# Optimization experiments

Measured on AMD Instinct MI355X. Metric: run time of the kernel, lower is better.

Reference implementation:

```python
import jax, jax.numpy as jnp
import numpy as np
from jax import lax

HEADS = 8
WIN_SIZES = (2, 4, 8)


def _linear(x, w, b):
    return x @ w + b


def _window_attention(x2d, ws, w4, b4):
    # x2d: (B,H,W,C); w4: (4,C,C) = [q,k,v,out]; b4: (4,C)
    B, H, W, C = x2d.shape
    p1, p2 = H // ws, W // ws
    xw = x2d.reshape(B, p1, ws, p2, ws, C).transpose(0, 1, 3, 2, 4, 5)
    xw = xw.reshape(B, p1, p2, ws * ws, C)
    hs = C // HEADS
    q = _linear(xw, w4[0], b4[0]).reshape(B, p1, p2, ws * ws, HEADS, hs)
    k = _linear(xw, w4[1], b4[1]).reshape(B, p1, p2, ws * ws, HEADS, hs)
    v = _linear(xw, w4[2], b4[2]).reshape(B, p1, p2, ws * ws, HEADS, hs)
    scores = jnp.einsum('bpqwhd,bpqvhd->bpqhwv', q, k) / jnp.sqrt(jnp.asarray(hs, x2d.dtype))
    probs = jax.nn.softmax(scores, axis=-1)
    ctx = jnp.einsum('bpqhwv,bpqvhd->bpqwhd', probs, v).reshape(B, p1, p2, ws * ws, C)
    return _linear(ctx, w4[3], b4[3])


def _unwindow(out, ws):
    B, p1, p2, win, C = out.shape
    s = out.reshape(B, p1, p2, ws, ws, C).transpose(0, 1, 3, 2, 4, 5)
    return s.reshape(B, p1 * ws, p2 * ws, C)


def _up_bilinear_ac(x, oh, ow):
    # x: (B,C,h,w); bilinear with align_corners=True (UpsamplingBilinear2d)
    B, C, h, w = x.shape
    def grid(o, i):
        pos = jnp.arange(o, dtype=x.dtype) * ((i - 1) / (o - 1))
        i0 = jnp.floor(pos).astype(jnp.int32)
        i1 = jnp.minimum(i0 + 1, i - 1)
        return i0, i1, pos - i0.astype(x.dtype)
    r0, r1, tr = grid(oh, h)
    c0, c1, tc = grid(ow, w)
    xr = x[:, :, r0, :] * (1 - tr)[None, None, :, None] + x[:, :, r1, :] * tr[None, None, :, None]
    return xr[:, :, :, c0] * (1 - tc) + xr[:, :, :, c1] * tc


def _forward(x, attn_w, attn_b, edge_w, mlp_w1, mlp_b1, mlp_w2, mlp_b2,
             dl_w, dl_b, ax_w, ax_b, g_shift, g_bias, sq_w, sq_b):
    B, N, C = x.shape
    H = W = int(np.sqrt(N))
    x2d = x.reshape(B, H, W, C)

    # multi-scale window attention branches
    scale_outputs = [_unwindow(_window_attention(x2d, ws, attn_w[i], attn_b[i]), ws)
                     for i, ws in enumerate(WIN_SIZES)]

    # adaptive window selector
    xc = x2d.transpose(0, 3, 1, 2)  # (B,C,H,W)
    edge = jnp.abs(lax.conv_general_dilated(xc, edge_w, (1, 1), 'SAME'))
    avg = lax.reduce_window(edge, 0.0, lax.add, (1, 1, 3, 3), (1, 1, 1, 1), 'SAME') / 9.0
    e = avg.transpose(0, 2, 3, 1)  # (B,H,W,1)
    wts = jax.nn.softmax(jax.nn.relu(e @ mlp_w1 + mlp_b1) @ mlp_w2 + mlp_b2, axis=-1)

    blended = sum(wts[..., i:i + 1] * scale_outputs[i] for i in range(len(WIN_SIZES)))
    h_map = blended.transpose(0, 3, 1, 2)  # (B,C,H,W)

    # ws=4 window attention -> DlightConv token pooling
    x_win = _window_attention(x2d, 4, attn_w[1], attn_b[1])  # (B,p,p,16,C)
    probs = jax.nn.softmax(jnp.mean(x_win, axis=-2) @ dl_w + dl_b, axis=-1)
    x_dl = jnp.sum(x_win * probs[..., None], axis=-2)  # (B,p,p,C)

    # axial attention (no head split, no scaling in the axial branch)
    q = _linear(x_dl, ax_w[0], ax_b[0])
    k = _linear(x_dl, ax_w[1], ax_b[1])
    v = _linear(x_dl, ax_w[2], ax_b[2])
    scores_x = jnp.einsum('bhwc,bhvc->bhwv', q, k)  # (B,r,c,k)
    scores_y = jnp.einsum('bhwc,bvwc->bwhv', q, k)  # (B,c,r,k)

    # GaussianTrans: vectorized per-pixel gaussian positional bias
    p = x_dl.shape[1]
    idx = jnp.arange(p, dtype=x.dtype)
    dist2 = (idx[None, :] - idx[:, None]) ** 2          # [pos, k]
    gb = -(g_shift[0] * dist2 + g_bias[0])              # (p,p)
    ax = jax.nn.softmax(scores_x + gb[None, None, :, :], axis=-1)       # bias indexed by c
    ay = jax.nn.softmax(jnp.swapaxes(scores_y, 1, 2) + gb[None, :, None, :], axis=-1)  # bias by r
    x_g = jnp.einsum('brck,brkd->brcd', ax, v) + jnp.einsum('brck,bkcd->brcd', ay, v)

    x_g = _up_bilinear_ac(x_g.transpose(0, 3, 1, 2), H, W)  # (B,C,H,W)

    cat = jnp.concatenate([x_g, h_map], axis=1)  # (B,2C,H,W)
    out = jnp.einsum('oc,bchw->bohw', sq_w, cat) + sq_b[None, :, None, None]
    return out.transpose(0, 2, 3, 1).reshape(B, N, C)


def setup_inputs() -> dict:
    key = jax.random.key(0)
    ks = jax.random.split(key, 16)
    B, N, C = 16, 4096, 256
    s = 0.02
    return {
        'x': jax.random.normal(ks[0], (B, N, C), jnp.float32),
        'attn_w': jax.random.normal(ks[1], (3, 4, C, C), jnp.float32) * s,
        'attn_b': jax.random.normal(ks[2], (3, 4, C), jnp.float32) * s,
        'edge_w': jax.random.normal(ks[3], (1, C, 3, 3), jnp.float32) * s,
        'mlp_w1': jax.random.normal(ks[4], (1, 16), jnp.float32) * s,
        'mlp_b1': jax.random.normal(ks[5], (16,), jnp.float32) * s,
        'mlp_w2': jax.random.normal(ks[6], (16, 3), jnp.float32) * s,
        'mlp_b2': jax.random.normal(ks[7], (3,), jnp.float32) * s,
        'dl_w': jax.random.normal(ks[8], (C, 16), jnp.float32) * s,
        'dl_b': jax.random.normal(ks[9], (16,), jnp.float32) * s,
        'ax_w': jax.random.normal(ks[10], (3, C, C), jnp.float32) * s,
        'ax_b': jax.random.normal(ks[11], (3, C), jnp.float32) * s,
        'g_shift': jnp.abs(jax.random.normal(ks[12], (1,), jnp.float32)),
        'g_bias': -jnp.abs(jax.random.normal(ks[13], (1,), jnp.float32)),
        'sq_w': jax.random.normal(ks[14], (C, 2 * C), jnp.float32) * s,
        'sq_b': jax.random.normal(ks[15], (C,), jnp.float32) * s,
    }


def reference(x, attn_w, attn_b, edge_w, mlp_w1, mlp_b1, mlp_w2, mlp_b2,
              dl_w, dl_b, ax_w, ax_b, g_shift, g_bias, sq_w, sq_b):
    return _forward(x, attn_w, attn_b, edge_w, mlp_w1, mlp_b1, mlp_w2, mlp_b2,
                    dl_w, dl_b, ax_w, ax_b, g_shift, g_bias, sq_w, sq_b)
```

## Files before the change

### kernel.cpp

```cpp
#include <hip/hip_runtime.h>
#include <math.h>


#define CHUNK_B 4
#define CHUNK_TOK (CHUNK_B * 4096)
#define SA 40

typedef __attribute__((ext_vector_type(8))) short short8;
typedef __attribute__((ext_vector_type(4))) float f32x4;

__device__ __forceinline__ ushort f2bf(float f) {
    union { float f; unsigned u; } v; v.f = f;
    unsigned r = v.u + 0x7fff + ((v.u >> 16) & 1);
    return (ushort)(r >> 16);
}
__device__ __forceinline__ float bf2f(ushort h) {
    union { unsigned u; float f; } v; v.u = ((unsigned)h) << 16; return v.f;
}
__device__ __forceinline__ void split2(float v, ushort& h, ushort& l) {
    h = f2bf(v);
    l = f2bf(v - bf2f(h));
}

__global__ __launch_bounds__(256) void split_w_kmajor(
    const float* __restrict__ W, ushort* __restrict__ Th, ushort* __restrict__ Tl, int nmats)
{
    const int idx = blockIdx.x * 256 + threadIdx.x;
    if (idx >= nmats * 65536) return;
    const int mat = idx >> 16, r = idx & 65535;
    const int n = r >> 8, k = r & 255;
    const float v = W[(size_t)mat * 65536 + k * 256 + n];
    ushort h, l; split2(v, h, l);
    Th[idx] = h; Tl[idx] = l;
}
__global__ __launch_bounds__(256) void split_w_nmajor(
    const float* __restrict__ W, ushort* __restrict__ Th, ushort* __restrict__ Tl, int total)
{
    const int idx = blockIdx.x * 256 + threadIdx.x;
    if (idx >= total) return;
    ushort h, l; split2(W[idx], h, l);
    Th[idx] = h; Tl[idx] = l;
}


#define GEMM_DECLS                                                            \
    __shared__ ushort Ah[128 * SA], Al[128 * SA], Bh[128 * SA], Bl[128 * SA]; \
    const int tid = threadIdx.x;                                              \
    const int wave = tid >> 6, lane = tid & 63;                               \
    const int quad = lane >> 4, l16 = lane & 15;                              \
    const int wr = (wave >> 1) * 64, wc = (wave & 1) * 64;                    \
    f32x4 acc[4][4];                                                          \
    _Pragma("unroll") for (int i = 0; i < 4; i++)                             \
        _Pragma("unroll") for (int j = 0; j < 4; j++)                         \
            acc[i][j] = (f32x4){0.f, 0.f, 0.f, 0.f};                          \
    const int srow = tid >> 1;                                    \
    const int skp  = (tid & 1) * 16;

#define STAGE_A(Aptr, kk)                                                     \
    {                                                                         \
        const float* src = (Aptr) + (size_t)(m0 + srow) * 256 + (kk) + skp;   \
        _Pragma("unroll") for (int c = 0; c < 4; c++) {                       \
            float4 v = *(const float4*)(src + c * 4);                         \
            ushort4 h, l;                                                     \
            split2(v.x, h.x, l.x); split2(v.y, h.y, l.y);                     \
            split2(v.z, h.z, l.z); split2(v.w, h.w, l.w);                     \
            *(ushort4*)&Ah[srow * SA + skp + c * 4] = h;                      \
            *(ushort4*)&Al[srow * SA + skp + c * 4] = l;                      \
        }                                                                     \
    }

#define STAGE_B(WthP, WtlP, Kst, k0)                                          \
    {                                                                         \
        const size_t wo = (size_t)(srow) * (Kst) + (k0) + skp;                \
        *(ulonglong2*)&Bh[srow * SA + skp]     = *(const ulonglong2*)((WthP) + wo);     \
        *(ulonglong2*)&Bh[srow * SA + skp + 8] = *(const ulonglong2*)((WthP) + wo + 8); \
        *(ulonglong2*)&Bl[srow * SA + skp]     = *(const ulonglong2*)((WtlP) + wo);     \
        *(ulonglong2*)&Bl[srow * SA + skp + 8] = *(const ulonglong2*)((WtlP) + wo + 8); \
    }

#define GEMM_COMPUTE                                                          \
    {                                                                         \
        short8 afh[4], afl[4], bfh[4], bfl[4];                                \
        _Pragma("unroll") for (int i = 0; i < 4; i++) {                       \
            const int ro = (wr + i * 16 + l16) * SA + quad * 8;               \
            afh[i] = *(const short8*)&Ah[ro];                                 \
            afl[i] = *(const short8*)&Al[ro];                                 \
        }                                                                     \
        _Pragma("unroll") for (int j = 0; j < 4; j++) {                       \
            const int no = (wc + j * 16 + l16) * SA + quad * 8;               \
            bfh[j] = *(const short8*)&Bh[no];                                 \
            bfl[j] = *(const short8*)&Bl[no];                                 \
        }                                                                     \
        _Pragma("unroll") for (int i = 0; i < 4; i++)                         \
            _Pragma("unroll") for (int j = 0; j < 4; j++) {                   \
                acc[i][j] = __builtin_amdgcn_mfma_f32_16x16x32_bf16(          \
                    afh[i], bfh[j], acc[i][j], 0, 0, 0);                      \
                acc[i][j] = __builtin_amdgcn_mfma_f32_16x16x32_bf16(          \
                    afl[i], bfh[j], acc[i][j], 0, 0, 0);                      \
                acc[i][j] = __builtin_amdgcn_mfma_f32_16x16x32_bf16(          \
                    afh[i], bfl[j], acc[i][j], 0, 0, 0);                      \
            }                                                                 \
    }

__global__ __launch_bounds__(256, 2) void gemm3_mfma(
    const float* __restrict__ A,
    const ushort* __restrict__ Wth, const ushort* __restrict__ Wtl,
    const float* __restrict__ b0, const float* __restrict__ b1, const float* __restrict__ b2,
    float* __restrict__ O0, float* __restrict__ O1, float* __restrict__ O2)
{
    const int m0 = blockIdx.x * 128;
    const int mat = blockIdx.y >> 1;
    const int col0 = (blockIdx.y & 1) * 128;
    const ushort* wth = Wth + (size_t)mat * 65536 + (size_t)col0 * 256;
    const ushort* wtl = Wtl + (size_t)mat * 65536 + (size_t)col0 * 256;
    GEMM_DECLS
    for (int k0 = 0; k0 < 256; k0 += 32) {
        STAGE_A(A, k0)
        STAGE_B(wth, wtl, 256, k0)
        __syncthreads();
        GEMM_COMPUTE
        __syncthreads();
    }
    const float* bias = (mat == 0) ? b0 : (mat == 1) ? b1 : b2;
    float* O = (mat == 0) ? O0 : (mat == 1) ? O1 : O2;
#pragma unroll
    for (int j = 0; j < 4; j++) {
        const int col = col0 + wc + j * 16 + l16;
        const float bj = bias[col];
#pragma unroll
        for (int i = 0; i < 4; i++) {
            const int rbase = m0 + wr + i * 16 + quad * 4;
#pragma unroll
            for (int r = 0; r < 4; r++)
                O[(size_t)(rbase + r) * 256 + col] = acc[i][j][r] + bj;
        }
    }
}

__global__ __launch_bounds__(256, 2) void gemmp_mfma(
    const float* __restrict__ A,
    const ushort* __restrict__ Wth, const ushort* __restrict__ Wtl,
    const float* __restrict__ bias,
    float* __restrict__ Sout, int store_s,
    float* __restrict__ Blnd, const float* __restrict__ wts, int scale_idx, int blend_init,
    int row_off)
{
    const int m0 = blockIdx.x * 128;
    const int col0 = blockIdx.y * 128;
    const ushort* wth = Wth + (size_t)col0 * 256;
    const ushort* wtl = Wtl + (size_t)col0 * 256;
    GEMM_DECLS
    for (int k0 = 0; k0 < 256; k0 += 32) {
        STAGE_A(A, k0)
        STAGE_B(wth, wtl, 256, k0)
        __syncthreads();
        GEMM_COMPUTE
        __syncthreads();
    }
#pragma unroll
    for (int i = 0; i < 4; i++) {
        const int rbase = m0 + wr + i * 16 + quad * 4;
#pragma unroll
        for (int r = 0; r < 4; r++) {
            const size_t grow = (size_t)row_off + rbase + r;
            const float wt = wts[grow * 3 + scale_idx];
#pragma unroll
            for (int j = 0; j < 4; j++) {
                const int col = col0 + wc + j * 16 + l16;
                const float v = acc[i][j][r] + bias[col];
                if (store_s) Sout[grow * 256 + col] = v;
                float* bp = Blnd + grow * 256 + col;
                if (blend_init) *bp = wt * v;
                else            *bp = *bp + wt * v;
            }
        }
    }
}

__global__ __launch_bounds__(256, 2) void gemmf_mfma(
    const float* __restrict__ UP, const float* __restrict__ BLD,
    const ushort* __restrict__ Wth, const ushort* __restrict__ Wtl,
    const float* __restrict__ SQB, float* __restrict__ OUT)
{
    const int m0 = blockIdx.x * 128;
    const int col0 = blockIdx.y * 128;
    const ushort* wth = Wth + (size_t)col0 * 512;
    const ushort* wtl = Wtl + (size_t)col0 * 512;
    GEMM_DECLS
    for (int k0 = 0; k0 < 512; k0 += 32) {
        const float* Ap = (k0 < 256) ? UP : BLD;
        STAGE_A(Ap, (k0 & 255))
        STAGE_B(wth, wtl, 512, k0)
        __syncthreads();
        GEMM_COMPUTE
        __syncthreads();
    }
#pragma unroll
    for (int j = 0; j < 4; j++) {
        const int col = col0 + wc + j * 16 + l16;
        const float bj = SQB[col];
#pragma unroll
        for (int i = 0; i < 4; i++) {
            const int rbase = m0 + wr + i * 16 + quad * 4;
#pragma unroll
            for (int r = 0; r < 4; r++)
                OUT[(size_t)(rbase + r) * 256 + col] = acc[i][j][r] + bj;
        }
    }
}

template <int WS, int NH>
__global__ __launch_bounds__(256) void win_attn(
    const float* __restrict__ Q, const float* __restrict__ K,
    const float* __restrict__ V, float* __restrict__ CTX)
{
    constexpr int WIN = WS * WS;
    constexpr int NW = 64 / WS;
    constexpr int CW = NH * 32;
    __shared__ float qs[WIN][CW + 4], ks[WIN][CW + 4], vs[WIN][CW + 4];
    __shared__ float sc[NH][WIN][WIN + 1];
    const int tid = threadIdx.x;
    const int wid = blockIdx.x;
    const int b = wid / (NW * NW);
    const int rem = wid % (NW * NW);
    const int p = rem / NW, q = rem % NW;
    const int h0 = blockIdx.y * NH;

    for (int idx = tid; idx < WIN * CW; idx += 256) {
        const int i = idx / CW;
        const int cc = idx % CW;
        const int ti = i / WS, tj = i % WS;
        const size_t g = ((size_t)(b * 4096 + (p * WS + ti) * 64 + (q * WS + tj))) * 256 + h0 * 32 + cc;
        qs[i][cc] = Q[g]; ks[i][cc] = K[g]; vs[i][cc] = V[g];
    }
    __syncthreads();
    const float scale = 0.17677669529663687f;
    for (int idx = tid; idx < NH * WIN * WIN; idx += 256) {
        const int hl = idx / (WIN * WIN);
        const int r = idx % (WIN * WIN);
        const int i = r / WIN, j = r % WIN;
        const int co = hl * 32;
        float s = 0.f;
#pragma unroll
        for (int d = 0; d < 32; d++) s += qs[i][co + d] * ks[j][co + d];
        sc[hl][i][j] = s * scale;
    }
    __syncthreads();
    if (tid < NH * WIN) {
        const int hl = tid / WIN, i = tid % WIN;
        float mx = -3.4e38f;
        for (int j = 0; j < WIN; j++) mx = fmaxf(mx, sc[hl][i][j]);
        float sum = 0.f;
        for (int j = 0; j < WIN; j++) {
            float e = __expf(sc[hl][i][j] - mx);
            sc[hl][i][j] = e; sum += e;
        }
        const float inv = 1.f / sum;
        for (int j = 0; j < WIN; j++) sc[hl][i][j] *= inv;
    }
    __syncthreads();
    for (int idx = tid; idx < WIN * CW; idx += 256) {
        const int i = idx / CW;
        const int cc = idx % CW;
        const int hl = cc >> 5;
        float s = 0.f;
        for (int j = 0; j < WIN; j++) s += sc[hl][i][j] * vs[j][cc];
        const int ti = i / WS, tj = i % WS;
        const size_t g = ((size_t)(b * 4096 + (p * WS + ti) * 64 + (q * WS + tj))) * 256 + h0 * 32 + cc;
        CTX[g] = s;
    }
}

__global__ __launch_bounds__(256) void edge_conv(
    const float* __restrict__ x, const float* __restrict__ ew, float* __restrict__ edge)
{
    __shared__ float wsm[2304];
    __shared__ float red[4];
    const int bh = blockIdx.x;
    const int b = bh >> 6, h = bh & 63;
    const int tid = threadIdx.x;
    for (int i = tid; i < 2304; i += 256) wsm[i] = ew[i];
    __syncthreads();
    float wc[9];
#pragma unroll
    for (int t = 0; t < 9; t++) wc[t] = wsm[tid * 9 + t];

    for (int w = 0; w < 64; w++) {
        float acc = 0.f;
#pragma unroll
        for (int kh = 0; kh < 3; kh++) {
            const int hh = h + kh - 1;
            if ((unsigned)hh > 63u) continue;
#pragma unroll
            for (int kw = 0; kw < 3; kw++) {
                const int ww = w + kw - 1;
                if ((unsigned)ww > 63u) continue;
                acc += x[((size_t)b * 4096 + hh * 64 + ww) * 256 + tid] * wc[kh * 3 + kw];
            }
        }
        for (int off = 32; off; off >>= 1) acc += __shfl_down(acc, off);
        if ((tid & 63) == 0) red[tid >> 6] = acc;
        __syncthreads();
        if (tid == 0)
            edge[(size_t)b * 4096 + h * 64 + w] = fabsf(red[0] + red[1] + red[2] + red[3]);
        __syncthreads();
    }
}

__global__ __launch_bounds__(256) void avg_mlp(
    const float* __restrict__ edge, const float* __restrict__ w1, const float* __restrict__ b1,
    const float* __restrict__ w2, const float* __restrict__ b2, float* __restrict__ wts)
{
    const int idx = blockIdx.x * 256 + threadIdx.x;
    const int b = idx >> 12, rem = idx & 4095, h = rem >> 6, w = rem & 63;
    float s = 0.f;
#pragma unroll
    for (int kh = -1; kh <= 1; kh++) {
        const int hh = h + kh;
        if ((unsigned)hh > 63u) continue;
#pragma unroll
        for (int kw = -1; kw <= 1; kw++) {
            const int ww = w + kw;
            if ((unsigned)ww > 63u) continue;
            s += edge[(size_t)b * 4096 + hh * 64 + ww];
        }
    }
    const float e = s / 9.f;
    float l0 = b2[0], l1 = b2[1], l2 = b2[2];
#pragma unroll
    for (int j = 0; j < 16; j++) {
        float hd = fmaxf(e * w1[j] + b1[j], 0.f);
        l0 += hd * w2[j * 3 + 0];
        l1 += hd * w2[j * 3 + 1];
        l2 += hd * w2[j * 3 + 2];
    }
    const float mx = fmaxf(l0, fmaxf(l1, l2));
    const float e0 = __expf(l0 - mx), e1 = __expf(l1 - mx), e2 = __expf(l2 - mx);
    const float inv = 1.f / (e0 + e1 + e2);
    wts[(size_t)idx * 3 + 0] = e0 * inv;
    wts[(size_t)idx * 3 + 1] = e1 * inv;
    wts[(size_t)idx * 3 + 2] = e2 * inv;
}

__global__ __launch_bounds__(256) void dlight(
    const float* __restrict__ S1, const float* __restrict__ dlw,
    const float* __restrict__ dlb, float* __restrict__ XDL)
{
    __shared__ float xw[16][257];
    __shared__ float m[256];
    __shared__ float pr[16];
    __shared__ float pr2[16];
    const int wid = blockIdx.x;
    const int b = wid >> 8, rem = wid & 255, p = rem >> 4, q = rem & 15;
    const int tid = threadIdx.x;
#pragma unroll
    for (int t = 0; t < 16; t++) {
        const int ti = t >> 2, tj = t & 3;
        xw[t][tid] = S1[((size_t)b * 4096 + (p * 4 + ti) * 64 + (q * 4 + tj)) * 256 + tid];
    }
    float mm = 0.f;
#pragma unroll
    for (int t = 0; t < 16; t++) mm += xw[t][tid];
    m[tid] = mm * (1.f / 16.f);
    __syncthreads();
    if (tid < 16) {
        float lg = dlb[tid];
        for (int c = 0; c < 256; c++) lg += m[c] * dlw[c * 16 + tid];
        pr[tid] = lg;
    }
    __syncthreads();
    if (tid < 16) {
        float mx = -3.4e38f;
        for (int j = 0; j < 16; j++) mx = fmaxf(mx, pr[j]);
        float sum = 0.f;
        for (int j = 0; j < 16; j++) sum += __expf(pr[j] - mx);
        pr2[tid] = __expf(pr[tid] - mx) / sum;
    }
    __syncthreads();
    float o = 0.f;
#pragma unroll
    for (int t = 0; t < 16; t++) o += xw[t][tid] * pr2[t];
    XDL[(size_t)wid * 256 + tid] = o;
}

__global__ __launch_bounds__(256) void axial_row(
    const float* __restrict__ Q, const float* __restrict__ K, const float* __restrict__ V,
    const float* __restrict__ gsp, const float* __restrict__ gbp, float* __restrict__ XG)
{
    __shared__ float qs[16][257], ks[16][257], vs[16][257];
    __shared__ float sc[16][17];
    const int bid = blockIdx.x;
    const int b = bid >> 4, r = bid & 15;
    const int tid = threadIdx.x;
    const float gs = gsp[0], gb = gbp[0];
#pragma unroll
    for (int w = 0; w < 16; w++) {
        const size_t base = ((size_t)b * 256 + r * 16 + w) * 256 + tid;
        qs[w][tid] = Q[base]; ks[w][tid] = K[base]; vs[w][tid] = V[base];
    }
    __syncthreads();
    {
        const int w = tid >> 4, vv = tid & 15;
        float s = 0.f;
        for (int c = 0; c < 256; c++) s += qs[w][c] * ks[vv][c];
        const float d = (float)(w - vv);
        sc[w][vv] = s - (gs * d * d + gb);
    }
    __syncthreads();
    if (tid < 16) {
        float mx = -3.4e38f;
        for (int j = 0; j < 16; j++) mx = fmaxf(mx, sc[tid][j]);
        float sum = 0.f;
        for (int j = 0; j < 16; j++) {
            float e = __expf(sc[tid][j] - mx);
            sc[tid][j] = e; sum += e;
        }
        const float inv = 1.f / sum;
        for (int j = 0; j < 16; j++) sc[tid][j] *= inv;
    }
    __syncthreads();
#pragma unroll
    for (int w2 = 0; w2 < 16; w2++) {
        float o = 0.f;
#pragma unroll
        for (int k2 = 0; k2 < 16; k2++) o += sc[w2][k2] * vs[k2][tid];
        XG[((size_t)b * 256 + r * 16 + w2) * 256 + tid] = o;
    }
}

__global__ __launch_bounds__(256) void axial_col(
    const float* __restrict__ Q, const float* __restrict__ K, const float* __restrict__ V,
    const float* __restrict__ gsp, const float* __restrict__ gbp, float* __restrict__ XG)
{
    __shared__ float qs[16][257], ks[16][257], vs[16][257];
    __shared__ float sc[16][17];
    const int bid = blockIdx.x;
    const int b = bid >> 4, col = bid & 15;
    const int tid = threadIdx.x;
    const float gs = gsp[0], gb = gbp[0];
#pragma unroll
    for (int h = 0; h < 16; h++) {
        const size_t base = ((size_t)b * 256 + h * 16 + col) * 256 + tid;
        qs[h][tid] = Q[base]; ks[h][tid] = K[base]; vs[h][tid] = V[base];
    }
    __syncthreads();
    {
        const int r = tid >> 4, vv = tid & 15;
        float s = 0.f;
        for (int c = 0; c < 256; c++) s += qs[r][c] * ks[vv][c];
        const float d = (float)(r - vv);
        sc[r][vv] = s - (gs * d * d + gb);
    }
    __syncthreads();
    if (tid < 16) {
        float mx = -3.4e38f;
        for (int j = 0; j < 16; j++) mx = fmaxf(mx, sc[tid][j]);
        float sum = 0.f;
        for (int j = 0; j < 16; j++) {
            float e = __expf(sc[tid][j] - mx);
            sc[tid][j] = e; sum += e;
        }
        const float inv = 1.f / sum;
        for (int j = 0; j < 16; j++) sc[tid][j] *= inv;
    }
    __syncthreads();
#pragma unroll
    for (int r2 = 0; r2 < 16; r2++) {
        float o = 0.f;
#pragma unroll
        for (int k2 = 0; k2 < 16; k2++) o += sc[r2][k2] * vs[k2][tid];
        XG[((size_t)b * 256 + r2 * 16 + col) * 256 + tid] += o;
    }
}

__global__ __launch_bounds__(256) void upsample(
    const float* __restrict__ XG, float* __restrict__ UP)
{
    const unsigned idx = blockIdx.x * 256u + threadIdx.x;
    const int c = idx & 255;
    const unsigned t2 = idx >> 8;
    const int w = t2 & 63;
    const unsigned t3 = t2 >> 6;
    const int h = t3 & 63;
    const int b = t3 >> 6;
    const float rr = 15.f / 63.f;
    const float ph = h * rr, pw = w * rr;
    int h0 = (int)floorf(ph); float th = ph - (float)h0; int h1 = min(h0 + 1, 15);
    int w0 = (int)floorf(pw); float tw = pw - (float)w0; int w1 = min(w0 + 1, 15);
    const size_t bb = (size_t)b * 256;
    const float v00 = XG[((bb + h0 * 16 + w0)) * 256 + c];
    const float v10 = XG[((bb + h1 * 16 + w0)) * 256 + c];
    const float v01 = XG[((bb + h0 * 16 + w1)) * 256 + c];
    const float v11 = XG[((bb + h1 * 16 + w1)) * 256 + c];
    const float c0 = v00 * (1.f - th) + v10 * th;
    const float c1 = v01 * (1.f - th) + v11 * th;
    UP[idx] = c0 * (1.f - tw) + c1 * tw;
}

extern "C" void kernel_launch(void* const* d_in, const int* in_sizes, int n_in,
                              void* d_out, int out_size, void* d_ws, size_t ws_size,
                              hipStream_t stream)
{
    const float* x      = (const float*)d_in[0];
    const float* attn_w = (const float*)d_in[1];
    const float* attn_b = (const float*)d_in[2];
    const float* edge_w = (const float*)d_in[3];
    const float* mlp_w1 = (const float*)d_in[4];
    const float* mlp_b1 = (const float*)d_in[5];
    const float* mlp_w2 = (const float*)d_in[6];
    const float* mlp_b2 = (const float*)d_in[7];
    const float* dl_w   = (const float*)d_in[8];
    const float* dl_b   = (const float*)d_in[9];
    const float* ax_w   = (const float*)d_in[10];
    const float* ax_b   = (const float*)d_in[11];
    const float* g_shift= (const float*)d_in[12];
    const float* g_bias = (const float*)d_in[13];
    const float* sq_w   = (const float*)d_in[14];
    const float* sq_b   = (const float*)d_in[15];
    float* out = (float*)d_out;

    float* ws = (float*)d_ws;
    const size_t MT = 65536;
    float* blend = ws;
    float* s1    = blend + MT * 256;
    float* scr   = s1 + MT * 256;
    float* chQ   = scr;
    float* chK   = chQ + (size_t)CHUNK_TOK * 256;
    float* chV   = chK + (size_t)CHUNK_TOK * 256;
    float* up    = scr;
    float* edge  = scr + MT * 256;
    float* wts   = edge + 65536;
    float* xdl   = wts + 196608;
    float* axq   = xdl + 1048576;
    float* axk   = axq + 1048576;
    float* axv   = axk + 1048576;
    float* xg    = axv + 1048576;
    ushort* Wth = (ushort*)(xg + 1048576);
    ushort* Wtl = Wth + 1114112;

    split_w_kmajor<<<(12 * 65536 + 255) / 256, 256, 0, stream>>>(attn_w, Wth, Wtl, 12);
    split_w_kmajor<<<(3 * 65536 + 255) / 256, 256, 0, stream>>>(
        ax_w, Wth + (size_t)12 * 65536, Wtl + (size_t)12 * 65536, 3);
    split_w_nmajor<<<(131072 + 255) / 256, 256, 0, stream>>>(
        sq_w, Wth + (size_t)15 * 65536, Wtl + (size_t)15 * 65536, 131072);

    edge_conv<<<1024, 256, 0, stream>>>(x, edge_w, edge);
    avg_mlp<<<256, 256, 0, stream>>>(edge, mlp_w1, mlp_b1, mlp_w2, mlp_b2, wts);

    for (int i = 0; i < 3; i++) {
        const ushort* Wh = Wth + (size_t)i * 4 * 65536;
        const ushort* Wl = Wtl + (size_t)i * 4 * 65536;
        const float* c0 = attn_b + (size_t)(i * 4 + 0) * 256;
        const float* c1 = attn_b + (size_t)(i * 4 + 1) * 256;
        const float* c2 = attn_b + (size_t)(i * 4 + 2) * 256;
        const float* c3 = attn_b + (size_t)(i * 4 + 3) * 256;
        for (int ch = 0; ch < 16 / CHUNK_B; ch++) {
            const size_t toff = (size_t)ch * CHUNK_TOK;
            const float* xc = x + toff * 256;
            gemm3_mfma<<<dim3(CHUNK_TOK / 128, 6), 256, 0, stream>>>(
                xc, Wh, Wl, c0, c1, c2, chQ, chK, chV);
            if (i == 0)
                win_attn<2, 8><<<dim3(CHUNK_B * 32 * 32, 1), 256, 0, stream>>>(chQ, chK, chV, chQ);
            if (i == 1)
                win_attn<4, 4><<<dim3(CHUNK_B * 16 * 16, 2), 256, 0, stream>>>(chQ, chK, chV, chQ);
            if (i == 2)
                win_attn<8, 1><<<dim3(CHUNK_B * 8 * 8, 8), 256, 0, stream>>>(chQ, chK, chV, chQ);
            gemmp_mfma<<<dim3(CHUNK_TOK / 128, 2), 256, 0, stream>>>(
                chQ, Wh + (size_t)3 * 65536, Wl + (size_t)3 * 65536, c3,
                s1, (i == 1) ? 1 : 0, blend, wts, i, (i == 0) ? 1 : 0, (int)toff);
        }
    }

    dlight<<<4096, 256, 0, stream>>>(s1, dl_w, dl_b, xdl);

    gemm3_mfma<<<dim3(4096 / 128, 6), 256, 0, stream>>>(
        xdl, Wth + (size_t)12 * 65536, Wtl + (size_t)12 * 65536,
        ax_b, ax_b + 256, ax_b + 512, axq, axk, axv);
    axial_row<<<256, 256, 0, stream>>>(axq, axk, axv, g_shift, g_bias, xg);
    axial_col<<<256, 256, 0, stream>>>(axq, axk, axv, g_shift, g_bias, xg);

    upsample<<<65536, 256, 0, stream>>>(xg, up);

    gemmf_mfma<<<dim3(512, 2), 256, 0, stream>>>(
        up, blend, Wth + (size_t)15 * 65536, Wtl + (size_t)15 * 65536, sq_b, out);
}
```

Measured before the change: 1.409 ms.

## Split edge conv into per-pixel channel contraction then 3x3 spatial combine

Replaces the edge-detection conv kernel, which looped over 64 columns per block with two block-wide barriers per output pixel, with two kernels. The first contracts each pixel's 256 channels against the 9 filter taps, so x is read once instead of up to nine times. The second sums the neighbouring tap values into the edge map. This removes the per-pixel syncthreads serialisation and the redundant reads, at the cost of a small intermediate buffer (9 floats per pixel) and one extra launch.

```diff
diff --git a/kernel.cpp b/kernel.cpp
--- a/kernel.cpp
+++ b/kernel.cpp
@@ -41,7 +41,6 @@
     ushort h, l; split2(W[idx], h, l);
     Th[idx] = h; Tl[idx] = l;
 }
-
 
 #define GEMM_DECLS                                                            \
     __shared__ ushort Ah[128 * SA], Al[128 * SA], Bh[128 * SA], Bl[128 * SA]; \
@@ -271,40 +270,64 @@
     }
 }
 
-__global__ __launch_bounds__(256) void edge_conv(
-    const float* __restrict__ x, const float* __restrict__ ew, float* __restrict__ edge)
+__global__ __launch_bounds__(256) void edge_gemm9(
+    const float* __restrict__ x, const float* __restrict__ ew, float* __restrict__ ytmp)
 {
     __shared__ float wsm[2304];
-    __shared__ float red[4];
-    const int bh = blockIdx.x;
-    const int b = bh >> 6, h = bh & 63;
     const int tid = threadIdx.x;
     for (int i = tid; i < 2304; i += 256) wsm[i] = ew[i];
     __syncthreads();
-    float wc[9];
-#pragma unroll
-    for (int t = 0; t < 9; t++) wc[t] = wsm[tid * 9 + t];
-
-    for (int w = 0; w < 64; w++) {
-        float acc = 0.f;
-#pragma unroll
-        for (int kh = 0; kh < 3; kh++) {
-            const int hh = h + kh - 1;
-            if ((unsigned)hh > 63u) continue;
-#pragma unroll
-            for (int kw = 0; kw < 3; kw++) {
-                const int ww = w + kw - 1;
-                if ((unsigned)ww > 63u) continue;
-                acc += x[((size_t)b * 4096 + hh * 64 + ww) * 256 + tid] * wc[kh * 3 + kw];
-            }
-        }
-        for (int off = 32; off; off >>= 1) acc += __shfl_down(acc, off);
-        if ((tid & 63) == 0) red[tid >> 6] = acc;
-        __syncthreads();
-        if (tid == 0)
-            edge[(size_t)b * 4096 + h * 64 + w] = fabsf(red[0] + red[1] + red[2] + red[3]);
-        __syncthreads();
-    }
+    const int wave = tid >> 6, lane = tid & 63;
+    const int p = blockIdx.x * 4 + wave;
+    const float4 xv = *(const float4*)(x + (size_t)p * 256 + lane * 4);
+    float acc[9];
+#pragma unroll
+    for (int t = 0; t < 9; t++) acc[t] = 0.f;
+    const float xs[4] = {xv.x, xv.y, xv.z, xv.w};
+#pragma unroll
+    for (int i = 0; i < 4; i++) {
+        const int c = lane * 4 + i;
+#pragma unroll
+        for (int t = 0; t < 9; t++)
+            acc[t] = fmaf(xs[i], wsm[c * 9 + t], acc[t]);
+    }
+#pragma unroll
+    for (int t = 0; t < 9; t++) {
+#pragma unroll
+        for (int off = 1; off < 64; off <<= 1)
+            acc[t] += __shfl_xor(acc[t], off);
+    }
+    if (lane < 9) {
+        float v = acc[0];
+        switch (lane) {
+            case 1: v = acc[1]; break; case 2: v = acc[2]; break;
+            case 3: v = acc[3]; break; case 4: v = acc[4]; break;
+            case 5: v = acc[5]; break; case 6: v = acc[6]; break;
+            case 7: v = acc[7]; break; case 8: v = acc[8]; break;
+            default: break;
+        }
+        ytmp[(size_t)p * 9 + lane] = v;
+    }
+}
+
+__global__ __launch_bounds__(256) void edge_combine(
+    const float* __restrict__ ytmp, float* __restrict__ edge)
+{
+    const int idx = blockIdx.x * 256 + threadIdx.x;
+    const int b = idx >> 12, rem = idx & 4095, h = rem >> 6, w = rem & 63;
+    float s = 0.f;
+#pragma unroll
+    for (int kh = 0; kh < 3; kh++) {
+        const int hh = h + kh - 1;
+        if ((unsigned)hh > 63u) continue;
+#pragma unroll
+        for (int kw = 0; kw < 3; kw++) {
+            const int ww = w + kw - 1;
+            if ((unsigned)ww > 63u) continue;
+            s += ytmp[((size_t)b * 4096 + hh * 64 + ww) * 9 + kh * 3 + kw];
+        }
+    }
+    edge[idx] = fabsf(s);
 }
 
 __global__ __launch_bounds__(256) void avg_mlp(
@@ -528,6 +551,7 @@
     float* chK   = chQ + (size_t)CHUNK_TOK * 256;
     float* chV   = chK + (size_t)CHUNK_TOK * 256;
     float* up    = scr;
+    float* ytmp  = scr;
     float* edge  = scr + MT * 256;
     float* wts   = edge + 65536;
     float* xdl   = wts + 196608;
@@ -544,7 +568,8 @@
     split_w_nmajor<<<(131072 + 255) / 256, 256, 0, stream>>>(
         sq_w, Wth + (size_t)15 * 65536, Wtl + (size_t)15 * 65536, 131072);
 
-    edge_conv<<<1024, 256, 0, stream>>>(x, edge_w, edge);
+    edge_gemm9<<<16384, 256, 0, stream>>>(x, edge_w, ytmp);
+    edge_combine<<<256, 256, 0, stream>>>(ytmp, edge);
     avg_mlp<<<256, 256, 0, stream>>>(edge, mlp_w1, mlp_b1, mlp_w2, mlp_b2, wts);
 
     for (int i = 0; i < 3; i++) {
```

Measured after the change: 1.299 ms. -7.8%, faster.
